# Kernel tuning notes

Hardware: AMD Instinct MI355X
Metric: run time of the kernel (lower is better)

The kernel has to match this reference:

```python
import jax, jax.numpy as jnp
import numpy as np

BS, P_PER = 4, 12000          # batch size, occupied pillars per sample
X_L, Y_L = 432, 496           # grid dims from point_cloud_range / voxel_size
N_PTS = 32                    # max_num_points per pillar


def setup_inputs() -> dict:
    key = jax.random.key(0)
    k1, k2 = jax.random.split(key)
    # torch) are deterministic and match jax .at[].set exactly.
    rng = np.random.default_rng(0)
    flat = np.stack([rng.choice(X_L * Y_L, size=P_PER, replace=False)
                     for _ in range(BS)])                    # (BS, P_PER)
    ix = (flat // Y_L).astype(np.int32)
    iy = (flat % Y_L).astype(np.int32)
    b = np.repeat(np.arange(BS, dtype=np.int32), P_PER)
    coors = jnp.asarray(np.stack([b, ix.ravel(), iy.ravel()], axis=1))  # (P, 3)
    pillars = jax.random.normal(k1, (BS * P_PER, N_PTS, 3), dtype=jnp.float32)
    npoints = jax.random.randint(k2, (BS * P_PER,), 1, N_PTS + 1, dtype=jnp.int32)
    return {"pillars": pillars, "coors": coors, "npoints": npoints}


def reference(pillars, coors, npoints):
    # pillars: (P, N, 3) voxelized points; coors: (P, 3) = (batch, ix, iy)
    # center of points per pillar: (P, 3)
    center = jnp.sum(pillars[:, :, :3], axis=1) / npoints[:, None].astype(pillars.dtype)
    b, ix, iy = coors[:, 0], coors[:, 1], coors[:, 2]
    n = pillars.shape[1]
    # dense scatter of all points: (BS, X_L, Y_L, N, 3) -> permute to (BS, 3, N, Y_L, X_L)
    pillar_all = jnp.zeros((BS, X_L, Y_L, n, 3), dtype=pillars.dtype)
    pillar_all = pillar_all.at[b, ix, iy].set(pillars[:, :, :3])
    pillar_all = jnp.transpose(pillar_all, (0, 4, 3, 2, 1))
    # dense scatter of centers: (BS, X_L, Y_L, 3) -> (BS, 3, Y_L, X_L)
    pillar_center = jnp.zeros((BS, X_L, Y_L, 3), dtype=pillars.dtype)
    pillar_center = pillar_center.at[b, ix, iy].set(center)
    pillar_center = jnp.transpose(pillar_center, (0, 3, 2, 1))
    return pillars, coors, npoints, pillar_all, pillar_center
```

## Files before the change

### kernel.cpp

```cpp
#include <hip/hip_runtime.h>

constexpr int BS = 4, P_PER = 12000, NP = BS * P_PER;
constexpr int XL = 432, YL = 496, NPTS = 32;
constexpr int XQ = XL / 4;
constexpr int NS = 3 * NPTS;
constexpr int YX = YL * XL;

constexpr long long SZ_P   = (long long)NP * NPTS * 3;
constexpr long long SZ_C   = (long long)NP * 3;
constexpr long long SZ_N   = NP;
constexpr long long SZ_ALL = (long long)BS * 3 * NPTS * YL * XL;
constexpr long long SZ_CTR = (long long)BS * 3 * YL * XL;

constexpr long long OFF_ALL = SZ_P + SZ_C + SZ_N;
constexpr long long OFF_CTR = OFF_ALL + SZ_ALL;

constexpr int MAXJ = 48;
constexpr int JCAP = 127;

typedef float nt4 __attribute__((ext_vector_type(4)));

constexpr int NB_ROW  = BS * YL;
constexpr int NB_CVT  = (int)((SZ_C / 4 + SZ_N / 4 + 255) / 256);
constexpr int NB_COPY = (int)(SZ_P / 4 / 256);
constexpr int NB_MEGA = NB_ROW + NB_CVT + NB_COPY;

__global__ __launch_bounds__(256) void build_map(const int* __restrict__ coors,
                                                 int* __restrict__ map)
{
    int p = blockIdx.x * 256 + threadIdx.x;
    if (p >= NP) return;
    int b  = coors[3 * p + 0];
    int ix = coors[3 * p + 1];
    int iy = coors[3 * p + 2];
    map[(b * YL + iy) * XL + ix] = p;
}

__global__ __launch_bounds__(256) void mega_kernel(
    const float* __restrict__ pillars, const int* __restrict__ coors,
    const int* __restrict__ npoints, const int* __restrict__ map,
    float* __restrict__ out)
{
    const int bid = blockIdx.x;
    const int t   = threadIdx.x;

    if (bid >= NB_ROW) {
        if (bid < NB_ROW + NB_CVT) {
            constexpr int NC = (int)(SZ_C / 4);
            constexpr int NN = (int)(SZ_N / 4);
            int u = (bid - NB_ROW) * 256 + t;
            if (u >= NC + NN) return;
            int4 a; long long dst;
            if (u < NC) { a = reinterpret_cast<const int4*>(coors)[u]; dst = SZ_P / 4 + u; }
            else { a = reinterpret_cast<const int4*>(npoints)[u - NC]; dst = SZ_P / 4 + NC + (u - NC); }
            nt4 o = {(float)a.x, (float)a.y, (float)a.z, (float)a.w};
            __builtin_nontemporal_store(o, reinterpret_cast<nt4*>(out) + dst);
        } else {
            long long u = (long long)(bid - NB_ROW - NB_CVT) * 256 + t;
            nt4 v = reinterpret_cast<const nt4*>(pillars)[u];
            __builtin_nontemporal_store(v, reinterpret_cast<nt4*>(out) + u);
        }
        return;
    }

    __shared__ float data[MAXJ][97];
    __shared__ float ctr[MAXJ * 3];
    __shared__ signed char col2j[XL];
    __shared__ int jlist[JCAP + 1];
    __shared__ int cnt;

    const int row = bid;
    const int b   = row / YL;
    const int iy  = row % YL;

    if (t == 0) cnt = 0;
    __syncthreads();

    const int* mrow = map + (b * YL + iy) * XL;
    for (int x = t; x < XL; x += 256) {
        int p = mrow[x];
        if (p >= 0) {
            int j = atomicAdd(&cnt, 1);
            if (j < JCAP) { jlist[j] = p; col2j[x] = (signed char)j; }
            else col2j[x] = -1;
        } else {
            col2j[x] = -1;
        }
    }
    __syncthreads();
    const int nOcc = (cnt < JCAP) ? cnt : JCAP;
    const int nChunks = (nOcc <= MAXJ) ? 1 : (nOcc + MAXJ - 1) / MAXJ;

    float* out_all = out + OFF_ALL + (long long)b * NS * YX + (long long)iy * XL;
    float* out_ctr = out + OFF_CTR + (long long)b * 3 * YX + (long long)iy * XL;

    for (int ch = 0; ch < nChunks; ++ch) {
        const int jbase = ch * MAXJ;
        int chunkN = nOcc - jbase;
        if (chunkN > MAXJ) chunkN = MAXJ;
        if (chunkN < 0) chunkN = 0;

        for (int i = t; i < chunkN * 24; i += 256) {
            int jl = i / 24, e4 = i % 24;
            float4 v = reinterpret_cast<const float4*>(pillars)
                           [(long long)jlist[jbase + jl] * 24 + e4];
            data[jl][e4 * 4 + 0] = v.x;
            data[jl][e4 * 4 + 1] = v.y;
            data[jl][e4 * 4 + 2] = v.z;
            data[jl][e4 * 4 + 3] = v.w;
        }
        __syncthreads();

        for (int i = t; i < chunkN * 3; i += 256) {
            int jl = i / 3, c = i % 3;
            float s = 0.f;
#pragma unroll
            for (int k = 0; k < NPTS; ++k) s += data[jl][k * 3 + c];
            ctr[i] = s / (float)npoints[jlist[jbase + jl]];
        }
        __syncthreads();

        if (ch == 0) {
            {
                int s = t / XQ;
                int q = t - s * XQ;
                float* pa = out_all + (long long)s * YX + (long long)q * 4;
                const unsigned int* cj4 = reinterpret_cast<const unsigned int*>(col2j);
                for (int i = t; i < NS * XQ; i += 256) {
                    int e = (s & 31) * 3 + (s >> 5);
                    unsigned int cc = cj4[q];
                    nt4 o;
                    int j0 = (int)(signed char)(cc & 0xff);
                    int j1 = (int)(signed char)((cc >> 8) & 0xff);
                    int j2 = (int)(signed char)((cc >> 16) & 0xff);
                    int j3 = (int)(signed char)(cc >> 24);
                    o.x = ((unsigned)j0 < MAXJ) ? data[j0][e] : 0.f;
                    o.y = ((unsigned)j1 < MAXJ) ? data[j1][e] : 0.f;
                    o.z = ((unsigned)j2 < MAXJ) ? data[j2][e] : 0.f;
                    o.w = ((unsigned)j3 < MAXJ) ? data[j3][e] : 0.f;
                    __builtin_nontemporal_store(o, reinterpret_cast<nt4*>(pa));
                    s += 2; q += 40;
                    long long step = 2LL * YX + 160;
                    if (q >= XQ) { q -= XQ; s += 1; step = 3LL * YX - 272; }
                    pa += step;
                }
            }
            {
                const unsigned int* cj4 = reinterpret_cast<const unsigned int*>(col2j);
                for (int i = t; i < 3 * XQ; i += 256) {
                    int c = i / XQ, q = i - c * XQ;
                    unsigned int cc = cj4[q];
                    nt4 o;
                    int j0 = (int)(signed char)(cc & 0xff);
                    int j1 = (int)(signed char)((cc >> 8) & 0xff);
                    int j2 = (int)(signed char)((cc >> 16) & 0xff);
                    int j3 = (int)(signed char)(cc >> 24);
                    o.x = ((unsigned)j0 < MAXJ) ? ctr[j0 * 3 + c] : 0.f;
                    o.y = ((unsigned)j1 < MAXJ) ? ctr[j1 * 3 + c] : 0.f;
                    o.z = ((unsigned)j2 < MAXJ) ? ctr[j2 * 3 + c] : 0.f;
                    o.w = ((unsigned)j3 < MAXJ) ? ctr[j3 * 3 + c] : 0.f;
                    __builtin_nontemporal_store(o,
                        reinterpret_cast<nt4*>(out_ctr + (long long)c * YX + q * 4));
                }
            }
        } else {
            for (int i = t; i < XL * NS; i += 256) {
                int x = i % XL, s = i / XL;
                int j = col2j[x];
                if (j >= jbase && j < jbase + chunkN) {
                    int e = (s & 31) * 3 + (s >> 5);
                    out_all[(long long)s * YX + x] = data[j - jbase][e];
                }
            }
            for (int i = t; i < XL * 3; i += 256) {
                int x = i % XL, c = i / XL;
                int j = col2j[x];
                if (j >= jbase && j < jbase + chunkN)
                    out_ctr[(long long)c * YX + x] = ctr[(j - jbase) * 3 + c];
            }
        }
        __syncthreads();
    }
}

__global__ __launch_bounds__(256) void scatter_kernel(
    const float* __restrict__ pillars, const int* __restrict__ coors,
    const int* __restrict__ npoints, float* __restrict__ out)
{
    int tid = blockIdx.x * blockDim.x + threadIdx.x;
    if (tid < NP * NPTS) {
        int p = tid / NPTS, k = tid % NPTS;
        int b = coors[3 * p], ix = coors[3 * p + 1], iy = coors[3 * p + 2];
#pragma unroll
        for (int c = 0; c < 3; ++c) {
            float val = pillars[(long long)p * 96 + k * 3 + c];
            long long e = OFF_ALL + ((((long long)(b * 3 + c) * NPTS + k) * YL + iy) * XL + ix);
            out[e] = val;
        }
    } else if (tid < NP * NPTS + NP) {
        int p = tid - NP * NPTS;
        int b = coors[3 * p], ix = coors[3 * p + 1], iy = coors[3 * p + 2];
        const float4* src = reinterpret_cast<const float4*>(pillars + (long long)p * 96);
        float s[3] = {0.f, 0.f, 0.f};
#pragma unroll
        for (int i = 0; i < 24; ++i) {
            float4 q = src[i];
            s[(4 * i + 0) % 3] += q.x;
            s[(4 * i + 1) % 3] += q.y;
            s[(4 * i + 2) % 3] += q.z;
            s[(4 * i + 3) % 3] += q.w;
        }
        float inv = 1.0f / (float)npoints[p];
#pragma unroll
        for (int c = 0; c < 3; ++c) {
            long long e = OFF_CTR + (((long long)(b * 3 + c) * YL + iy) * XL + ix);
            out[e] = s[c] * inv;
        }
    }
}

__global__ __launch_bounds__(256) void smallcvt_kernel(
    const int* __restrict__ coors, const int* __restrict__ npoints,
    float* __restrict__ out)
{
    constexpr int NC = (int)(SZ_C / 4);
    constexpr int NN = (int)(SZ_N / 4);
    int u = blockIdx.x * 256 + threadIdx.x;
    if (u >= NC + NN) return;
    int4 a; long long dst;
    if (u < NC) { a = reinterpret_cast<const int4*>(coors)[u]; dst = SZ_P / 4 + u; }
    else { a = reinterpret_cast<const int4*>(npoints)[u - NC]; dst = SZ_P / 4 + NC + (u - NC); }
    reinterpret_cast<float4*>(out)[dst] =
        float4{(float)a.x, (float)a.y, (float)a.z, (float)a.w};
}

extern "C" void kernel_launch(void* const* d_in, const int* in_sizes, int n_in,
                              void* d_out, int out_size, void* d_ws, size_t ws_size,
                              hipStream_t stream) {
    const float* pillars = (const float*)d_in[0];
    const int*   coors   = (const int*)d_in[1];
    const int*   npoints = (const int*)d_in[2];
    float*       out     = (float*)d_out;

    const size_t mapBytes = (size_t)BS * YL * XL * sizeof(int);

    if (ws_size >= mapBytes) {
        int* map = (int*)d_ws;
        (void)hipMemsetAsync(map, 0xFF, mapBytes, stream);
        build_map<<<(NP + 255) / 256, 256, 0, stream>>>(coors, map);
        mega_kernel<<<NB_MEGA, 256, 0, stream>>>(pillars, coors, npoints, map, out);
    } else {
        (void)hipMemcpyAsync(out, pillars, (size_t)SZ_P * sizeof(float),
                             hipMemcpyDeviceToDevice, stream);
        (void)hipMemsetAsync(out + OFF_ALL, 0, (size_t)(SZ_ALL + SZ_CTR) * sizeof(float), stream);
        smallcvt_kernel<<<(int)((SZ_C / 4 + SZ_N / 4 + 255) / 256), 256, 0, stream>>>(
            coors, npoints, out);
        int nthr = NP * NPTS + NP;
        scatter_kernel<<<(nthr + 255) / 256, 256, 0, stream>>>(pillars, coors, npoints, out);
    }
}
```

Baseline: 89.37 us.

## Restructure row scatter into per-wave slices with occupied-quad lists

Each wave now owns 24 consecutive output slices, and lanes map to fixed 4-column quads. A bitmask of occupied quads and a compact list of them are built once per row. Empty quads get plain zero stores, while the gather from shared memory runs only for occupied quads, with per-lane offsets hoisted out of the slice loop. Later chunks write directly at the occupied columns through a new column list instead of scanning all 432 columns. The aim is to cut per-store index arithmetic and shared-memory reads in a write-bound kernel, at the cost of more shared state and extra atomics during setup.

```diff
diff --git a/kernel.cpp b/kernel.cpp
--- a/kernel.cpp
+++ b/kernel.cpp
@@ -17,6 +17,7 @@
 
 constexpr int MAXJ = 48;
 constexpr int JCAP = 127;
+constexpr int OUCAP = 112;
 
 typedef float nt4 __attribute__((ext_vector_type(4)));
 
@@ -67,13 +68,18 @@
     __shared__ float ctr[MAXJ * 3];
     __shared__ signed char col2j[XL];
     __shared__ int jlist[JCAP + 1];
-    __shared__ int cnt;
-
-    const int row = bid;
-    const int b   = row / YL;
-    const int iy  = row % YL;
-
-    if (t == 0) cnt = 0;
+    __shared__ unsigned short occx[JCAP + 1];
+    __shared__ unsigned short occu[OUCAP];
+    __shared__ unsigned int ubit[4];
+    __shared__ int cnt, nou;
+
+    const int b    = bid / YL;
+    const int iy   = bid % YL;
+    const int wave = t >> 6;
+    const int lane = t & 63;
+
+    if (t == 0) { cnt = 0; nou = 0; }
+    if (t < 4) ubit[t] = 0;
     __syncthreads();
 
     const int* mrow = map + (b * YL + iy) * XL;
@@ -81,8 +87,10 @@
         int p = mrow[x];
         if (p >= 0) {
             int j = atomicAdd(&cnt, 1);
-            if (j < JCAP) { jlist[j] = p; col2j[x] = (signed char)j; }
-            else col2j[x] = -1;
+            if (j < JCAP) {
+                jlist[j] = p; occx[j] = (unsigned short)x;
+                col2j[x] = (signed char)j;
+            } else col2j[x] = -1;
         } else {
             col2j[x] = -1;
         }
@@ -91,8 +99,19 @@
     const int nOcc = (cnt < JCAP) ? cnt : JCAP;
     const int nChunks = (nOcc <= MAXJ) ? 1 : (nOcc + MAXJ - 1) / MAXJ;
 
+    if (t < XQ) {
+        unsigned int cc = reinterpret_cast<const unsigned int*>(col2j)[t];
+        if (cc != 0xFFFFFFFFu) {
+            int idx = atomicAdd(&nou, 1);
+            if (idx < OUCAP) occu[idx] = (unsigned short)t;
+            atomicOr(&ubit[t >> 5], 1u << (t & 31));
+        }
+    }
+
     float* out_all = out + OFF_ALL + (long long)b * NS * YX + (long long)iy * XL;
     float* out_ctr = out + OFF_CTR + (long long)b * 3 * YX + (long long)iy * XL;
+    const float* dflat = &data[0][0];
+    const nt4 z4 = {0.f, 0.f, 0.f, 0.f};
 
     for (int ch = 0; ch < nChunks; ++ch) {
         const int jbase = ch * MAXJ;
@@ -121,63 +140,100 @@
         __syncthreads();
 
         if (ch == 0) {
+            const int ua = lane, ub = lane + 64;
+            const bool za = !((ubit[ua >> 5] >> (ua & 31)) & 1u);
+            const bool zb = (ub < XQ) && !((ubit[ub >> 5] >> (ub & 31)) & 1u);
+            const int nouC = (nou < OUCAP) ? nou : OUCAP;
+            const bool act = lane < nouC;
+            const int  uo  = act ? (int)occu[lane] : 0;
+            const unsigned int cc = act
+                ? reinterpret_cast<const unsigned int*>(col2j)[uo] : 0xFFFFFFFFu;
+            const int j0 = (int)(signed char)(cc & 0xff);
+            const int j1 = (int)(signed char)((cc >> 8) & 0xff);
+            const int j2 = (int)(signed char)((cc >> 16) & 0xff);
+            const int j3 = (int)(signed char)(cc >> 24);
+            const bool v0 = (unsigned)j0 < (unsigned)MAXJ;
+            const bool v1 = (unsigned)j1 < (unsigned)MAXJ;
+            const bool v2 = (unsigned)j2 < (unsigned)MAXJ;
+            const bool v3 = (unsigned)j3 < (unsigned)MAXJ;
+            const int a0 = (v0 ? j0 : 0) * 97;
+            const int a1 = (v1 ? j1 : 0) * 97;
+            const int a2 = (v2 ? j2 : 0) * 97;
+            const int a3 = (v3 ? j3 : 0) * 97;
+
             {
-                int s = t / XQ;
-                int q = t - s * XQ;
-                float* pa = out_all + (long long)s * YX + (long long)q * 4;
-                const unsigned int* cj4 = reinterpret_cast<const unsigned int*>(col2j);
-                for (int i = t; i < NS * XQ; i += 256) {
-                    int e = (s & 31) * 3 + (s >> 5);
-                    unsigned int cc = cj4[q];
-                    nt4 o;
-                    int j0 = (int)(signed char)(cc & 0xff);
-                    int j1 = (int)(signed char)((cc >> 8) & 0xff);
-                    int j2 = (int)(signed char)((cc >> 16) & 0xff);
-                    int j3 = (int)(signed char)(cc >> 24);
-                    o.x = ((unsigned)j0 < MAXJ) ? data[j0][e] : 0.f;
-                    o.y = ((unsigned)j1 < MAXJ) ? data[j1][e] : 0.f;
-                    o.z = ((unsigned)j2 < MAXJ) ? data[j2][e] : 0.f;
-                    o.w = ((unsigned)j3 < MAXJ) ? data[j3][e] : 0.f;
-                    __builtin_nontemporal_store(o, reinterpret_cast<nt4*>(pa));
-                    s += 2; q += 40;
-                    long long step = 2LL * YX + 160;
-                    if (q >= XQ) { q -= XQ; s += 1; step = 3LL * YX - 272; }
-                    pa += step;
+                float* rowp = out_all + (long long)(wave * 24) * YX;
+                for (int s = wave * 24, send = s + 24; s < send; ++s, rowp += YX) {
+                    const int e = (s & 31) * 3 + (s >> 5);
+                    if (za) __builtin_nontemporal_store(z4, reinterpret_cast<nt4*>(rowp) + ua);
+                    if (zb) __builtin_nontemporal_store(z4, reinterpret_cast<nt4*>(rowp) + ub);
+                    if (act) {
+                        nt4 o;
+                        o.x = v0 ? dflat[a0 + e] : 0.f;
+                        o.y = v1 ? dflat[a1 + e] : 0.f;
+                        o.z = v2 ? dflat[a2 + e] : 0.f;
+                        o.w = v3 ? dflat[a3 + e] : 0.f;
+                        __builtin_nontemporal_store(o, reinterpret_cast<nt4*>(rowp) + uo);
+                    }
+                }
+                if (nouC > 64) {
+                    for (int s = wave * 24, send = s + 24; s < send; ++s) {
+                        const int e = (s & 31) * 3 + (s >> 5);
+                        float* rp = out_all + (long long)s * YX;
+                        for (int l = 64 + lane; l < nouC; l += 64) {
+                            int uu = occu[l];
+                            unsigned int c2 = reinterpret_cast<const unsigned int*>(col2j)[uu];
+                            nt4 o;
+                            int k0 = (int)(signed char)(c2 & 0xff);
+                            int k1 = (int)(signed char)((c2 >> 8) & 0xff);
+                            int k2 = (int)(signed char)((c2 >> 16) & 0xff);
+                            int k3 = (int)(signed char)(c2 >> 24);
+                            o.x = ((unsigned)k0 < MAXJ) ? data[k0][e] : 0.f;
+                            o.y = ((unsigned)k1 < MAXJ) ? data[k1][e] : 0.f;
+                            o.z = ((unsigned)k2 < MAXJ) ? data[k2][e] : 0.f;
+                            o.w = ((unsigned)k3 < MAXJ) ? data[k3][e] : 0.f;
+                            __builtin_nontemporal_store(o, reinterpret_cast<nt4*>(rp) + uu);
+                        }
+                    }
                 }
             }
-            {
-                const unsigned int* cj4 = reinterpret_cast<const unsigned int*>(col2j);
-                for (int i = t; i < 3 * XQ; i += 256) {
-                    int c = i / XQ, q = i - c * XQ;
-                    unsigned int cc = cj4[q];
+            if (wave < 3) {
+                float* rowp = out_ctr + (long long)wave * YX;
+                if (za) __builtin_nontemporal_store(z4, reinterpret_cast<nt4*>(rowp) + ua);
+                if (zb) __builtin_nontemporal_store(z4, reinterpret_cast<nt4*>(rowp) + ub);
+                if (act) {
                     nt4 o;
-                    int j0 = (int)(signed char)(cc & 0xff);
-                    int j1 = (int)(signed char)((cc >> 8) & 0xff);
-                    int j2 = (int)(signed char)((cc >> 16) & 0xff);
-                    int j3 = (int)(signed char)(cc >> 24);
-                    o.x = ((unsigned)j0 < MAXJ) ? ctr[j0 * 3 + c] : 0.f;
-                    o.y = ((unsigned)j1 < MAXJ) ? ctr[j1 * 3 + c] : 0.f;
-                    o.z = ((unsigned)j2 < MAXJ) ? ctr[j2 * 3 + c] : 0.f;
-                    o.w = ((unsigned)j3 < MAXJ) ? ctr[j3 * 3 + c] : 0.f;
-                    __builtin_nontemporal_store(o,
-                        reinterpret_cast<nt4*>(out_ctr + (long long)c * YX + q * 4));
+                    o.x = v0 ? ctr[j0 * 3 + wave] : 0.f;
+                    o.y = v1 ? ctr[j1 * 3 + wave] : 0.f;
+                    o.z = v2 ? ctr[j2 * 3 + wave] : 0.f;
+                    o.w = v3 ? ctr[j3 * 3 + wave] : 0.f;
+                    __builtin_nontemporal_store(o, reinterpret_cast<nt4*>(rowp) + uo);
+                }
+                if (nouC > 64) {
+                    for (int l = 64 + lane; l < nouC; l += 64) {
+                        int uu = occu[l];
+                        unsigned int c2 = reinterpret_cast<const unsigned int*>(col2j)[uu];
+                        nt4 o;
+                        int k0 = (int)(signed char)(c2 & 0xff);
+                        int k1 = (int)(signed char)((c2 >> 8) & 0xff);
+                        int k2 = (int)(signed char)((c2 >> 16) & 0xff);
+                        int k3 = (int)(signed char)(c2 >> 24);
+                        o.x = ((unsigned)k0 < MAXJ) ? ctr[k0 * 3 + wave] : 0.f;
+                        o.y = ((unsigned)k1 < MAXJ) ? ctr[k1 * 3 + wave] : 0.f;
+                        o.z = ((unsigned)k2 < MAXJ) ? ctr[k2 * 3 + wave] : 0.f;
+                        o.w = ((unsigned)k3 < MAXJ) ? ctr[k3 * 3 + wave] : 0.f;
+                        __builtin_nontemporal_store(o, reinterpret_cast<nt4*>(rowp) + uu);
+                    }
                 }
             }
         } else {
-            for (int i = t; i < XL * NS; i += 256) {
-                int x = i % XL, s = i / XL;
-                int j = col2j[x];
-                if (j >= jbase && j < jbase + chunkN) {
-                    int e = (s & 31) * 3 + (s >> 5);
-                    out_all[(long long)s * YX + x] = data[j - jbase][e];
-                }
+            for (int s = wave * 24, send = s + 24; s < send; ++s) {
+                const int e = (s & 31) * 3 + (s >> 5);
+                if (lane < chunkN)
+                    out_all[(long long)s * YX + occx[jbase + lane]] = data[lane][e];
             }
-            for (int i = t; i < XL * 3; i += 256) {
-                int x = i % XL, c = i / XL;
-                int j = col2j[x];
-                if (j >= jbase && j < jbase + chunkN)
-                    out_ctr[(long long)c * YX + x] = ctr[(j - jbase) * 3 + c];
-            }
+            if (wave < 3 && lane < chunkN)
+                out_ctr[(long long)wave * YX + occx[jbase + lane]] = ctr[lane * 3 + wave];
         }
         __syncthreads();
     }
```

Measured after the change: 199.3 us. 2.23x slower.

## Stage pillars into compacted plane-major buffer, then stream dense planes per window

Applied to the files above, without the earlier changes.

Adds a row-compaction pass that counts occupied cells per row, computes prefix offsets, and writes pillar points and centers into a transposed plane-major workspace buffer with 99 planes. A separate bigfill kernel then writes each output plane window with contiguous streaming stores, looking up values through a per-quad bitmask plus base index. This replaces the per-row mega kernel, whose strided writes across 96 planes per block were the main cost. It adds an extra kernel launch, workspace traffic and a serial prefix sum over preceding rows inside rowfill. The old scatter fallback for small workspaces is removed, so with too little workspace nothing runs.

```diff
diff --git a/kernel.cpp b/kernel.cpp
--- a/kernel.cpp
+++ b/kernel.cpp
@@ -5,6 +5,7 @@
 constexpr int XQ = XL / 4;
 constexpr int NS = 3 * NPTS;
 constexpr int YX = YL * XL;
+constexpr int NROW = BS * YL;
 
 constexpr long long SZ_P   = (long long)NP * NPTS * 3;
 constexpr long long SZ_C   = (long long)NP * 3;
@@ -15,25 +16,201 @@
 constexpr long long OFF_ALL = SZ_P + SZ_C + SZ_N;
 constexpr long long OFF_CTR = OFF_ALL + SZ_ALL;
 
-constexpr int MAXJ = 48;
-constexpr int JCAP = 127;
-
 typedef float nt4 __attribute__((ext_vector_type(4)));
 
-constexpr int NB_ROW  = BS * YL;
+constexpr size_t WS_MAP   = 0;
+constexpr size_t WS_RCNT  = WS_MAP  + (size_t)NROW * XL * 4;
+constexpr size_t WS_RMAP2 = WS_RCNT + (size_t)NROW * 4;
+constexpr size_t WS_PW    = WS_RMAP2 + (size_t)NROW * XQ * 8;
+constexpr size_t WS_NEED  = WS_PW + (size_t)99 * NP * 4;
+
+constexpr int PWLD = NP;
+constexpr int MAXJ = 64;
+constexpr int PCAP = 128;
+
+constexpr int NWIN    = YL / 16;
+constexpr int NB_ALL  = BS * NS * NWIN;
+constexpr int NB_CTR  = BS * 3 * NWIN;
 constexpr int NB_CVT  = (int)((SZ_C / 4 + SZ_N / 4 + 255) / 256);
 constexpr int NB_COPY = (int)(SZ_P / 4 / 256);
-constexpr int NB_MEGA = NB_ROW + NB_CVT + NB_COPY;
-
-__global__ __launch_bounds__(256) void build_map(const int* __restrict__ coors,
-                                                 int* __restrict__ map)
+constexpr int NB_BIG  = NB_ALL + NB_CTR + NB_CVT + NB_COPY;
+
+__global__ __launch_bounds__(256) void build_map2(const int* __restrict__ coors,
+                                                  int* __restrict__ map,
+                                                  int* __restrict__ rowcnt)
 {
     int p = blockIdx.x * 256 + threadIdx.x;
     if (p >= NP) return;
     int b  = coors[3 * p + 0];
     int ix = coors[3 * p + 1];
     int iy = coors[3 * p + 2];
-    map[(b * YL + iy) * XL + ix] = p;
+    int row = b * YL + iy;
+    map[row * XL + ix] = p;
+    atomicAdd(&rowcnt[row], 1);
+}
+
+static __device__ __forceinline__ int pfx(const unsigned int* bm, int x) {
+    int w = x >> 5, r = 0;
+    for (int i = 0; i < w; ++i) r += __popc(bm[i]);
+    r += __popc(bm[w] & ((1u << (x & 31)) - 1u));
+    return r;
+}
+
+__global__ __launch_bounds__(256) void rowfill(
+    const float* __restrict__ pillars, const int* __restrict__ npoints,
+    const int* __restrict__ map, const int* __restrict__ rowcnt,
+    uint2* __restrict__ rmap2, float* __restrict__ pw)
+{
+    __shared__ float data[MAXJ][97];
+    __shared__ float ctrv[MAXJ * 3];
+    __shared__ unsigned int bmap[14];
+    __shared__ int plist[PCAP];
+    __shared__ int rbase_sh;
+
+    const int row = blockIdx.x;
+    const int t   = threadIdx.x;
+    const int lane = t & 63;
+
+    if (t < 14) bmap[t] = 0;
+    if (t == 0) rbase_sh = 0;
+    __syncthreads();
+
+    const int* mrow = map + row * XL;
+    for (int x = t; x < XL; x += 256)
+        if (mrow[x] >= 0) atomicOr(&bmap[x >> 5], 1u << (x & 31));
+    int partial = 0;
+    for (int r = t; r < row; r += 256) partial += rowcnt[r];
+    for (int o = 32; o > 0; o >>= 1) partial += __shfl_down(partial, o);
+    if (lane == 0) atomicAdd(&rbase_sh, partial);
+    __syncthreads();
+    const int rbase = rbase_sh;
+
+    for (int x = t; x < XL; x += 256) {
+        int p = mrow[x];
+        if (p >= 0) {
+            int rl = pfx(bmap, x);
+            if (rl < PCAP) plist[rl] = p;
+        }
+    }
+    __syncthreads();
+
+    if (t < XQ) {
+        int x0 = 4 * t;
+        unsigned int m4 = (bmap[x0 >> 5] >> (x0 & 31)) & 0xFu;
+        rmap2[row * XQ + t] = uint2{(unsigned int)(rbase + pfx(bmap, x0)), m4};
+    }
+
+    int n = rowcnt[row];
+    if (n > PCAP) n = PCAP;
+    const int nChunks = (n + MAXJ - 1) / MAXJ;
+
+    for (int ch = 0; ch < nChunks; ++ch) {
+        const int jb = ch * MAXJ;
+        int cN = n - jb;
+        if (cN > MAXJ) cN = MAXJ;
+
+        for (int i = t; i < cN * 24; i += 256) {
+            int jl = i / 24, e4 = i % 24;
+            float4 v = reinterpret_cast<const float4*>(pillars)
+                           [(long long)plist[jb + jl] * 24 + e4];
+            data[jl][e4 * 4 + 0] = v.x;
+            data[jl][e4 * 4 + 1] = v.y;
+            data[jl][e4 * 4 + 2] = v.z;
+            data[jl][e4 * 4 + 3] = v.w;
+        }
+        __syncthreads();
+        for (int i = t; i < cN * 3; i += 256) {
+            int jl = i / 3, c = i % 3;
+            float s = 0.f;
+#pragma unroll
+            for (int k = 0; k < NPTS; ++k) s += data[jl][k * 3 + c];
+            ctrv[i] = s / (float)npoints[plist[jb + jl]];
+        }
+        __syncthreads();
+        for (int idx = t; idx < 99 * cN; idx += 256) {
+            int e = idx / cN, i = idx - e * cN;
+            float val = (e < 96) ? data[i][e] : ctrv[i * 3 + (e - 96)];
+            pw[(long long)e * PWLD + rbase + jb + i] = val;
+        }
+        __syncthreads();
+    }
+}
+
+__global__ __launch_bounds__(256) void bigfill(
+    const float* __restrict__ pillars, const int* __restrict__ coors,
+    const int* __restrict__ npoints, const uint2* __restrict__ rmap2,
+    const float* __restrict__ pw, float* __restrict__ out)
+{
+    const int bid = blockIdx.x;
+    const int t   = threadIdx.x;
+
+    if (bid < NB_ALL + NB_CTR) {
+        int e, iy0, b;
+        float* dst;
+        if (bid < NB_ALL) {
+            int w = bid % NWIN;
+            int s = (bid / NWIN) % NS;
+            b     = bid / (NWIN * NS);
+            e     = (s & 31) * 3 + (s >> 5);
+            iy0   = w * 16;
+            dst   = out + OFF_ALL + ((long long)(b * NS + s)) * YX + (long long)iy0 * XL;
+        } else {
+            int t2 = bid - NB_ALL;
+            int w = t2 % NWIN;
+            int c = (t2 / NWIN) % 3;
+            b     = t2 / (NWIN * 3);
+            e     = 96 + c;
+            iy0   = w * 16;
+            dst   = out + OFF_CTR + ((long long)(b * 3 + c)) * YX + (long long)iy0 * XL;
+        }
+        const uint2* rm = rmap2 + (b * YL + iy0) * XQ;
+        const float* pwe = pw + (long long)e * PWLD;
+        nt4* dst4 = reinterpret_cast<nt4*>(dst);
+        for (int u = t; u < 16 * XQ; u += 256) {
+            uint2 rv = rm[u];
+            nt4 o = {0.f, 0.f, 0.f, 0.f};
+            unsigned int m = rv.y;
+            if (m) {
+                unsigned int base = rv.x;
+                if (m & 1u) o.x = pwe[base];
+                if (m & 2u) o.y = pwe[base + __popc(m & 1u)];
+                if (m & 4u) o.z = pwe[base + __popc(m & 3u)];
+                if (m & 8u) o.w = pwe[base + __popc(m & 7u)];
+            }
+            __builtin_nontemporal_store(o, dst4 + u);
+        }
+        return;
+    }
+    if (bid < NB_ALL + NB_CTR + NB_CVT) {
+        constexpr int NC = (int)(SZ_C / 4);
+        constexpr int NN = (int)(SZ_N / 4);
+        int u = (bid - NB_ALL - NB_CTR) * 256 + t;
+        if (u >= NC + NN) return;
+        int4 a; long long dst;
+        if (u < NC) { a = reinterpret_cast<const int4*>(coors)[u]; dst = SZ_P / 4 + u; }
+        else { a = reinterpret_cast<const int4*>(npoints)[u - NC]; dst = SZ_P / 4 + NC + (u - NC); }
+        nt4 o = {(float)a.x, (float)a.y, (float)a.z, (float)a.w};
+        __builtin_nontemporal_store(o, reinterpret_cast<nt4*>(out) + dst);
+        return;
+    }
+    long long u = (long long)(bid - NB_ALL - NB_CTR - NB_CVT) * 256 + t;
+    nt4 v = reinterpret_cast<const nt4*>(pillars)[u];
+    __builtin_nontemporal_store(v, reinterpret_cast<nt4*>(out) + u);
+}
+
+constexpr int F_MAXJ = 48;
+constexpr int F_JCAP = 127;
+constexpr int F_NB_ROW  = NROW;
+constexpr int F_NB_CVT  = NB_CVT;
+constexpr int F_NB_COPY = NB_COPY;
+constexpr int F_NB_MEGA = F_NB_ROW + F_NB_CVT + F_NB_COPY;
+
+__global__ __launch_bounds__(256) void build_map(const int* __restrict__ coors,
+                                                 int* __restrict__ map)
+{
+    int p = blockIdx.x * 256 + threadIdx.x;
+    if (p >= NP) return;
+    map[(coors[3 * p] * YL + coors[3 * p + 2]) * XL + coors[3 * p + 1]] = p;
 }
 
 __global__ __launch_bounds__(256) void mega_kernel(
@@ -44,11 +221,11 @@
     const int bid = blockIdx.x;
     const int t   = threadIdx.x;
 
-    if (bid >= NB_ROW) {
-        if (bid < NB_ROW + NB_CVT) {
+    if (bid >= F_NB_ROW) {
+        if (bid < F_NB_ROW + F_NB_CVT) {
             constexpr int NC = (int)(SZ_C / 4);
             constexpr int NN = (int)(SZ_N / 4);
-            int u = (bid - NB_ROW) * 256 + t;
+            int u = (bid - F_NB_ROW) * 256 + t;
             if (u >= NC + NN) return;
             int4 a; long long dst;
             if (u < NC) { a = reinterpret_cast<const int4*>(coors)[u]; dst = SZ_P / 4 + u; }
@@ -56,22 +233,21 @@
             nt4 o = {(float)a.x, (float)a.y, (float)a.z, (float)a.w};
             __builtin_nontemporal_store(o, reinterpret_cast<nt4*>(out) + dst);
         } else {
-            long long u = (long long)(bid - NB_ROW - NB_CVT) * 256 + t;
+            long long u = (long long)(bid - F_NB_ROW - F_NB_CVT) * 256 + t;
             nt4 v = reinterpret_cast<const nt4*>(pillars)[u];
             __builtin_nontemporal_store(v, reinterpret_cast<nt4*>(out) + u);
         }
         return;
     }
 
-    __shared__ float data[MAXJ][97];
-    __shared__ float ctr[MAXJ * 3];
+    __shared__ float data[F_MAXJ][97];
+    __shared__ float ctr[F_MAXJ * 3];
     __shared__ signed char col2j[XL];
-    __shared__ int jlist[JCAP + 1];
+    __shared__ int jlist[F_JCAP + 1];
     __shared__ int cnt;
 
-    const int row = bid;
-    const int b   = row / YL;
-    const int iy  = row % YL;
+    const int b  = bid / YL;
+    const int iy = bid % YL;
 
     if (t == 0) cnt = 0;
     __syncthreads();
@@ -81,23 +257,21 @@
         int p = mrow[x];
         if (p >= 0) {
             int j = atomicAdd(&cnt, 1);
-            if (j < JCAP) { jlist[j] = p; col2j[x] = (signed char)j; }
+            if (j < F_JCAP) { jlist[j] = p; col2j[x] = (signed char)j; }
             else col2j[x] = -1;
-        } else {
-            col2j[x] = -1;
-        }
-    }
-    __syncthreads();
-    const int nOcc = (cnt < JCAP) ? cnt : JCAP;
-    const int nChunks = (nOcc <= MAXJ) ? 1 : (nOcc + MAXJ - 1) / MAXJ;
+        } else col2j[x] = -1;
+    }
+    __syncthreads();
+    const int nOcc = (cnt < F_JCAP) ? cnt : F_JCAP;
+    const int nChunks = (nOcc <= F_MAXJ) ? 1 : (nOcc + F_MAXJ - 1) / F_MAXJ;
 
     float* out_all = out + OFF_ALL + (long long)b * NS * YX + (long long)iy * XL;
     float* out_ctr = out + OFF_CTR + (long long)b * 3 * YX + (long long)iy * XL;
 
     for (int ch = 0; ch < nChunks; ++ch) {
-        const int jbase = ch * MAXJ;
+        const int jbase = ch * F_MAXJ;
         int chunkN = nOcc - jbase;
-        if (chunkN > MAXJ) chunkN = MAXJ;
+        if (chunkN > F_MAXJ) chunkN = F_MAXJ;
         if (chunkN < 0) chunkN = 0;
 
         for (int i = t; i < chunkN * 24; i += 256) {
@@ -110,7 +284,6 @@
             data[jl][e4 * 4 + 3] = v.w;
         }
         __syncthreads();
-
         for (int i = t; i < chunkN * 3; i += 256) {
             int jl = i / 3, c = i % 3;
             float s = 0.f;
@@ -134,10 +307,10 @@
                     int j1 = (int)(signed char)((cc >> 8) & 0xff);
                     int j2 = (int)(signed char)((cc >> 16) & 0xff);
                     int j3 = (int)(signed char)(cc >> 24);
-                    o.x = ((unsigned)j0 < MAXJ) ? data[j0][e] : 0.f;
-                    o.y = ((unsigned)j1 < MAXJ) ? data[j1][e] : 0.f;
-                    o.z = ((unsigned)j2 < MAXJ) ? data[j2][e] : 0.f;
-                    o.w = ((unsigned)j3 < MAXJ) ? data[j3][e] : 0.f;
+                    o.x = ((unsigned)j0 < F_MAXJ) ? data[j0][e] : 0.f;
+                    o.y = ((unsigned)j1 < F_MAXJ) ? data[j1][e] : 0.f;
+                    o.z = ((unsigned)j2 < F_MAXJ) ? data[j2][e] : 0.f;
+                    o.w = ((unsigned)j3 < F_MAXJ) ? data[j3][e] : 0.f;
                     __builtin_nontemporal_store(o, reinterpret_cast<nt4*>(pa));
                     s += 2; q += 40;
                     long long step = 2LL * YX + 160;
@@ -155,10 +328,10 @@
                     int j1 = (int)(signed char)((cc >> 8) & 0xff);
                     int j2 = (int)(signed char)((cc >> 16) & 0xff);
                     int j3 = (int)(signed char)(cc >> 24);
-                    o.x = ((unsigned)j0 < MAXJ) ? ctr[j0 * 3 + c] : 0.f;
-                    o.y = ((unsigned)j1 < MAXJ) ? ctr[j1 * 3 + c] : 0.f;
-                    o.z = ((unsigned)j2 < MAXJ) ? ctr[j2 * 3 + c] : 0.f;
-                    o.w = ((unsigned)j3 < MAXJ) ? ctr[j3 * 3 + c] : 0.f;
+                    o.x = ((unsigned)j0 < F_MAXJ) ? ctr[j0 * 3 + c] : 0.f;
+                    o.y = ((unsigned)j1 < F_MAXJ) ? ctr[j1 * 3 + c] : 0.f;
+                    o.z = ((unsigned)j2 < F_MAXJ) ? ctr[j2 * 3 + c] : 0.f;
+                    o.w = ((unsigned)j3 < F_MAXJ) ? ctr[j3 * 3 + c] : 0.f;
                     __builtin_nontemporal_store(o,
                         reinterpret_cast<nt4*>(out_ctr + (long long)c * YX + q * 4));
                 }
@@ -183,57 +356,6 @@
     }
 }
 
-__global__ __launch_bounds__(256) void scatter_kernel(
-    const float* __restrict__ pillars, const int* __restrict__ coors,
-    const int* __restrict__ npoints, float* __restrict__ out)
-{
-    int tid = blockIdx.x * blockDim.x + threadIdx.x;
-    if (tid < NP * NPTS) {
-        int p = tid / NPTS, k = tid % NPTS;
-        int b = coors[3 * p], ix = coors[3 * p + 1], iy = coors[3 * p + 2];
-#pragma unroll
-        for (int c = 0; c < 3; ++c) {
-            float val = pillars[(long long)p * 96 + k * 3 + c];
-            long long e = OFF_ALL + ((((long long)(b * 3 + c) * NPTS + k) * YL + iy) * XL + ix);
-            out[e] = val;
-        }
-    } else if (tid < NP * NPTS + NP) {
-        int p = tid - NP * NPTS;
-        int b = coors[3 * p], ix = coors[3 * p + 1], iy = coors[3 * p + 2];
-        const float4* src = reinterpret_cast<const float4*>(pillars + (long long)p * 96);
-        float s[3] = {0.f, 0.f, 0.f};
-#pragma unroll
-        for (int i = 0; i < 24; ++i) {
-            float4 q = src[i];
-            s[(4 * i + 0) % 3] += q.x;
-            s[(4 * i + 1) % 3] += q.y;
-            s[(4 * i + 2) % 3] += q.z;
-            s[(4 * i + 3) % 3] += q.w;
-        }
-        float inv = 1.0f / (float)npoints[p];
-#pragma unroll
-        for (int c = 0; c < 3; ++c) {
-            long long e = OFF_CTR + (((long long)(b * 3 + c) * YL + iy) * XL + ix);
-            out[e] = s[c] * inv;
-        }
-    }
-}
-
-__global__ __launch_bounds__(256) void smallcvt_kernel(
-    const int* __restrict__ coors, const int* __restrict__ npoints,
-    float* __restrict__ out)
-{
-    constexpr int NC = (int)(SZ_C / 4);
-    constexpr int NN = (int)(SZ_N / 4);
-    int u = blockIdx.x * 256 + threadIdx.x;
-    if (u >= NC + NN) return;
-    int4 a; long long dst;
-    if (u < NC) { a = reinterpret_cast<const int4*>(coors)[u]; dst = SZ_P / 4 + u; }
-    else { a = reinterpret_cast<const int4*>(npoints)[u - NC]; dst = SZ_P / 4 + NC + (u - NC); }
-    reinterpret_cast<float4*>(out)[dst] =
-        float4{(float)a.x, (float)a.y, (float)a.z, (float)a.w};
-}
-
 extern "C" void kernel_launch(void* const* d_in, const int* in_sizes, int n_in,
                               void* d_out, int out_size, void* d_ws, size_t ws_size,
                               hipStream_t stream) {
@@ -241,21 +363,22 @@
     const int*   coors   = (const int*)d_in[1];
     const int*   npoints = (const int*)d_in[2];
     float*       out     = (float*)d_out;
-
-    const size_t mapBytes = (size_t)BS * YL * XL * sizeof(int);
-
-    if (ws_size >= mapBytes) {
+    char*        ws      = (char*)d_ws;
+
+    if (ws_size >= WS_NEED) {
+        int*   map    = (int*)(ws + WS_MAP);
+        int*   rowcnt = (int*)(ws + WS_RCNT);
+        uint2* rmap2  = (uint2*)(ws + WS_RMAP2);
+        float* pw     = (float*)(ws + WS_PW);
+        (void)hipMemsetAsync(map, 0xFF, (size_t)NROW * XL * 4, stream);
+        (void)hipMemsetAsync(rowcnt, 0, (size_t)NROW * 4, stream);
+        build_map2<<<(NP + 255) / 256, 256, 0, stream>>>(coors, map, rowcnt);
+        rowfill<<<NROW, 256, 0, stream>>>(pillars, npoints, map, rowcnt, rmap2, pw);
+        bigfill<<<NB_BIG, 256, 0, stream>>>(pillars, coors, npoints, rmap2, pw, out);
+    } else if (ws_size >= (size_t)NROW * XL * 4) {
         int* map = (int*)d_ws;
-        (void)hipMemsetAsync(map, 0xFF, mapBytes, stream);
+        (void)hipMemsetAsync(map, 0xFF, (size_t)NROW * XL * 4, stream);
         build_map<<<(NP + 255) / 256, 256, 0, stream>>>(coors, map);
-        mega_kernel<<<NB_MEGA, 256, 0, stream>>>(pillars, coors, npoints, map, out);
-    } else {
-        (void)hipMemcpyAsync(out, pillars, (size_t)SZ_P * sizeof(float),
-                             hipMemcpyDeviceToDevice, stream);
-        (void)hipMemsetAsync(out + OFF_ALL, 0, (size_t)(SZ_ALL + SZ_CTR) * sizeof(float), stream);
-        smallcvt_kernel<<<(int)((SZ_C / 4 + SZ_N / 4 + 255) / 256), 256, 0, stream>>>(
-            coors, npoints, out);
-        int nthr = NP * NPTS + NP;
-        scatter_kernel<<<(nthr + 255) / 256, 256, 0, stream>>>(pillars, coors, npoints, out);
-    }
-}
+        mega_kernel<<<F_NB_MEGA, 256, 0, stream>>>(pillars, coors, npoints, map, out);
+    }
+}
```

Measured after the change: 103.9 us. 16.3% more time.
